# Kernel tuning notes

Measured on AMD Instinct MI355X. Metric: run time of the kernel, lower is better.

## Reference

```python
import jax, jax.numpy as jnp
import numpy as np

B, T, U = 4, 256, 128
ENC_H, PRED_H, JOINT_H = 512, 640, 640
NUM_CLASSES = 1024 + 1  # vocab + blank


def setup_inputs() -> dict:
    key = jax.random.key(0)
    ks = jax.random.split(key, 8)
    s = lambda fan_in: 1.0 / np.sqrt(fan_in)
    return {
        'encoder_outputs': jax.random.normal(ks[0], (B, ENC_H, T), jnp.float32),
        'decoder_outputs': jax.random.normal(ks[1], (B, PRED_H, U), jnp.float32),
        'W_enc': jax.random.uniform(ks[2], (JOINT_H, ENC_H), jnp.float32, -s(ENC_H), s(ENC_H)),
        'b_enc': jax.random.uniform(ks[3], (JOINT_H,), jnp.float32, -s(ENC_H), s(ENC_H)),
        'W_pred': jax.random.uniform(ks[4], (JOINT_H, PRED_H), jnp.float32, -s(PRED_H), s(PRED_H)),
        'b_pred': jax.random.uniform(ks[5], (JOINT_H,), jnp.float32, -s(PRED_H), s(PRED_H)),
        'W_joint': jax.random.uniform(ks[6], (NUM_CLASSES, JOINT_H), jnp.float32, -s(JOINT_H), s(JOINT_H)),
        'b_joint': jax.random.uniform(ks[7], (NUM_CLASSES,), jnp.float32, -s(JOINT_H), s(JOINT_H)),
    }


def reference(encoder_outputs, decoder_outputs, W_enc, b_enc, W_pred, b_pred, W_joint, b_joint):
    # encoder_outputs: [B, H_enc, T] -> [B, T, H_enc]; decoder: [B, H_pred, U] -> [B, U, H_pred]
    f = jnp.swapaxes(encoder_outputs, 1, 2)
    g = jnp.swapaxes(decoder_outputs, 1, 2)
    f = jnp.einsum('bth,jh->btj', f, W_enc) + b_enc          # [B, T, H]
    g = jnp.einsum('buh,jh->buj', g, W_pred) + b_pred        # [B, U, H]
    inp = f[:, :, None, :] + g[:, None, :, :]                # [B, T, U, H]
    hidden = jax.nn.relu(inp)
    logits = jnp.einsum('btuh,vh->btuv', hidden, W_joint) + b_joint  # [B, T, U, V+1]
    return jax.nn.log_softmax(logits, axis=-1)
```

## Files before the change

### kernel.cpp

```cpp
#include <hip/hip_runtime.h>

#define B_    4
#define T_    256
#define U_    128
#define ENC_H 512
#define PRED_H 640
#define JH    640
#define V_    1025
#define VMAIN 1024

#define BM    64
#define KC    32
#define APITCH 40
#define NKC   (JH / KC)

typedef float f32x4  __attribute__((ext_vector_type(4)));
typedef short bf16x8 __attribute__((ext_vector_type(8)));

__device__ __forceinline__ short bf16_rne(float x) {
    unsigned u = __float_as_uint(x);
    unsigned r = (u + 0x7fffu + ((u >> 16) & 1u)) >> 16;
    return (short)r;
}

__global__ __launch_bounds__(256) void proj_kernel(
    const float* __restrict__ X, const float* __restrict__ W,
    const float* __restrict__ bias, float* __restrict__ Y,
    int K, int M, int N)
{
    __shared__ float Xs[16][32];
    __shared__ float Ws[64][17];

    const int b  = blockIdx.z;
    const int m0 = blockIdx.x * 32;
    const int n0 = blockIdx.y * 64;
    const int tid = threadIdx.x;
    const int tx = tid & 15;
    const int ty = tid >> 4;

    const float* Xb = X + (size_t)b * K * M;

    float acc[2][4] = {{0.f,0.f,0.f,0.f},{0.f,0.f,0.f,0.f}};

    for (int k0 = 0; k0 < K; k0 += 16) {
        #pragma unroll
        for (int j = 0; j < 2; ++j) {
            int e = tid + j * 256;
            Xs[e >> 5][e & 31] = Xb[(size_t)(k0 + (e >> 5)) * M + m0 + (e & 31)];
        }
        #pragma unroll
        for (int j = 0; j < 4; ++j) {
            int e = tid + j * 256;
            Ws[e >> 4][e & 15] = W[(size_t)(n0 + (e >> 4)) * K + k0 + (e & 15)];
        }
        __syncthreads();
        #pragma unroll
        for (int k = 0; k < 16; ++k) {
            float a0 = Xs[k][ty * 2 + 0];
            float a1 = Xs[k][ty * 2 + 1];
            float b0 = Ws[tx * 4 + 0][k];
            float b1 = Ws[tx * 4 + 1][k];
            float b2 = Ws[tx * 4 + 2][k];
            float b3 = Ws[tx * 4 + 3][k];
            acc[0][0] += a0 * b0; acc[0][1] += a0 * b1;
            acc[0][2] += a0 * b2; acc[0][3] += a0 * b3;
            acc[1][0] += a1 * b0; acc[1][1] += a1 * b1;
            acc[1][2] += a1 * b2; acc[1][3] += a1 * b3;
        }
        __syncthreads();
    }

    #pragma unroll
    for (int i = 0; i < 2; ++i) {
        int m = m0 + ty * 2 + i;
        #pragma unroll
        for (int j = 0; j < 4; ++j) {
            int n = n0 + tx * 4 + j;
            Y[(size_t)(b * M + m) * N + n] = acc[i][j] + bias[n];
        }
    }
}

__global__ __launch_bounds__(256) void cvt_kernel(
    const float* __restrict__ W, short* __restrict__ o, int n)
{
    int i = blockIdx.x * 256 + threadIdx.x;
    if (i < n) o[i] = bf16_rne(W[i]);
}

__global__ __launch_bounds__(1024) void joint_kernel(
    const float* __restrict__ f,
    const float* __restrict__ g,
    const short* __restrict__ wj,
    const float* __restrict__ Wj32,
    const float* __restrict__ bj,
    float* __restrict__ out)
{
    __shared__ __align__(16) short As[2][BM * APITCH];
    __shared__ float red[BM][16];
    __shared__ float zp[BM][16];
    __shared__ float rowmax_s[BM], lse_s[BM], z1024_s[BM];

    const int bt = blockIdx.x >> 1;
    const int uh = blockIdx.x & 1;
    const int b  = bt >> 8;
    const int u0 = uh * BM;

    const float* frow = f + (size_t)bt * JH;
    const float* grow = g + (size_t)(b * U_ + u0) * JH;

    const int tid  = threadIdx.x;
    const int lane = tid & 63;
    const int wv   = tid >> 6;
    const int q    = lane >> 4;
    const int l15  = lane & 15;

    const int su = tid >> 4;
    const int sk = (tid & 15) * 2;

    f32x4 acc[4][4];
    #pragma unroll
    for (int rt = 0; rt < 4; ++rt)
        #pragma unroll
        for (int ct = 0; ct < 4; ++ct)
            acc[rt][ct] = (f32x4){0.f, 0.f, 0.f, 0.f};

    {
        float f0 = frow[sk], f1 = frow[sk + 1];
        float g0 = grow[su * JH + sk], g1 = grow[su * JH + sk + 1];
        As[0][su * APITCH + sk]     = bf16_rne(fmaxf(f0 + g0, 0.f));
        As[0][su * APITCH + sk + 1] = bf16_rne(fmaxf(f1 + g1, 0.f));
    }
    __syncthreads();

    for (int kc = 0; kc < NKC; ++kc) {
        const int cur = kc & 1;
        const bool more = (kc + 1) < NKC;
        float h0 = 0.f, h1 = 0.f;
        if (more) {
            const int k0n = (kc + 1) * KC;
            float f0 = frow[k0n + sk], f1 = frow[k0n + sk + 1];
            float g0 = grow[su * JH + k0n + sk], g1 = grow[su * JH + k0n + sk + 1];
            h0 = fmaxf(f0 + g0, 0.f);
            h1 = fmaxf(f1 + g1, 0.f);
        }
        const int k0 = kc * KC;
        bf16x8 bfr[4];
        #pragma unroll
        for (int ct = 0; ct < 4; ++ct) {
            const int col = (wv << 6) + (ct << 4) + l15;
            bfr[ct] = *(const bf16x8*)(wj + (size_t)col * JH + k0 + (q << 3));
        }
        bf16x8 afr[4];
        #pragma unroll
        for (int rt = 0; rt < 4; ++rt)
            afr[rt] = *(const bf16x8*)(&As[cur][(rt * 16 + l15) * APITCH + (q << 3)]);
        #pragma unroll
        for (int rt = 0; rt < 4; ++rt)
            #pragma unroll
            for (int ct = 0; ct < 4; ++ct)
                acc[rt][ct] = __builtin_amdgcn_mfma_f32_16x16x32_bf16(
                    afr[rt], bfr[ct], acc[rt][ct], 0, 0, 0);
        if (more) {
            const int ni = su * APITCH + sk;
            As[cur ^ 1][ni]     = bf16_rne(h0);
            As[cur ^ 1][ni + 1] = bf16_rne(h1);
        }
        __syncthreads();
    }

    float mloc[4][4];
    #pragma unroll
    for (int rt = 0; rt < 4; ++rt)
        #pragma unroll
        for (int r = 0; r < 4; ++r) mloc[rt][r] = -3.0e38f;

    #pragma unroll
    for (int ct = 0; ct < 4; ++ct) {
        const float bb = bj[(wv << 6) + (ct << 4) + l15];
        #pragma unroll
        for (int rt = 0; rt < 4; ++rt)
            #pragma unroll
            for (int r = 0; r < 4; ++r) {
                acc[rt][ct][r] += bb;
                mloc[rt][r] = fmaxf(mloc[rt][r], acc[rt][ct][r]);
            }
    }
    #pragma unroll
    for (int off = 1; off < 16; off <<= 1)
        #pragma unroll
        for (int rt = 0; rt < 4; ++rt)
            #pragma unroll
            for (int r = 0; r < 4; ++r)
                mloc[rt][r] = fmaxf(mloc[rt][r], __shfl_xor(mloc[rt][r], off));
    if (l15 == 0) {
        #pragma unroll
        for (int rt = 0; rt < 4; ++rt)
            #pragma unroll
            for (int r = 0; r < 4; ++r)
                red[rt * 16 + (q << 2) + r][wv] = mloc[rt][r];
    }
    {
        const int row  = tid >> 4;
        const int part = tid & 15;
        const float* w1024 = Wj32 + (size_t)VMAIN * JH;
        float s = 0.f;
        const int kb = part * 40;
        for (int kk = kb; kk < kb + 40; ++kk) {
            float h = fmaxf(frow[kk] + grow[row * JH + kk], 0.f);
            s += h * w1024[kk];
        }
        zp[row][part] = s;
    }
    __syncthreads();

    if (tid < BM) {
        float mx = red[tid][0];
        #pragma unroll
        for (int w = 1; w < 16; ++w) mx = fmaxf(mx, red[tid][w]);
        float z = bj[VMAIN];
        #pragma unroll
        for (int w = 0; w < 16; ++w) z += zp[tid][w];
        mx = fmaxf(mx, z);
        rowmax_s[tid] = mx;
        z1024_s[tid]  = z;
    }
    __syncthreads();

    float sloc[4][4];
    #pragma unroll
    for (int rt = 0; rt < 4; ++rt)
        #pragma unroll
        for (int r = 0; r < 4; ++r) {
            const float mx = rowmax_s[rt * 16 + (q << 2) + r];
            float s = 0.f;
            #pragma unroll
            for (int ct = 0; ct < 4; ++ct)
                s += __expf(acc[rt][ct][r] - mx);
            sloc[rt][r] = s;
        }
    #pragma unroll
    for (int off = 1; off < 16; off <<= 1)
        #pragma unroll
        for (int rt = 0; rt < 4; ++rt)
            #pragma unroll
            for (int r = 0; r < 4; ++r)
                sloc[rt][r] += __shfl_xor(sloc[rt][r], off);
    if (l15 == 0) {
        #pragma unroll
        for (int rt = 0; rt < 4; ++rt)
            #pragma unroll
            for (int r = 0; r < 4; ++r)
                red[rt * 16 + (q << 2) + r][wv] = sloc[rt][r];
    }
    __syncthreads();

    const size_t obase = (size_t)(bt * U_ + u0) * V_;
    if (tid < BM) {
        float tot = __expf(z1024_s[tid] - rowmax_s[tid]);
        #pragma unroll
        for (int w = 0; w < 16; ++w) tot += red[tid][w];
        float lse = rowmax_s[tid] + __logf(tot);
        lse_s[tid] = lse;
        out[obase + (size_t)tid * V_ + VMAIN] = z1024_s[tid] - lse;
    }
    __syncthreads();

    #pragma unroll
    for (int rt = 0; rt < 4; ++rt)
        #pragma unroll
        for (int r = 0; r < 4; ++r) {
            const int row = rt * 16 + (q << 2) + r;
            const float l = lse_s[row];
            #pragma unroll
            for (int ct = 0; ct < 4; ++ct) {
                const int col = (wv << 6) + (ct << 4) + l15;
                out[obase + (size_t)row * V_ + col] = acc[rt][ct][r] - l;
            }
        }
}

extern "C" void kernel_launch(void* const* d_in, const int* in_sizes, int n_in,
                              void* d_out, int out_size, void* d_ws, size_t ws_size,
                              hipStream_t stream) {
    const float* enc   = (const float*)d_in[0];
    const float* dec   = (const float*)d_in[1];
    const float* Wenc  = (const float*)d_in[2];
    const float* benc  = (const float*)d_in[3];
    const float* Wpred = (const float*)d_in[4];
    const float* bpred = (const float*)d_in[5];
    const float* Wj    = (const float*)d_in[6];
    const float* bjt   = (const float*)d_in[7];
    float* out = (float*)d_out;

    char* ws = (char*)d_ws;
    float* f_ws  = (float*)ws;
    float* g_ws  = (float*)(ws + 2621440);
    short* wj_ws = (short*)(ws + 2621440 + 1310720);

    proj_kernel<<<dim3(8, 10, 4), 256, 0, stream>>>(enc, Wenc, benc, f_ws, ENC_H, T_, JH);
    proj_kernel<<<dim3(4, 10, 4), 256, 0, stream>>>(dec, Wpred, bpred, g_ws, PRED_H, U_, JH);
    cvt_kernel<<<dim3((VMAIN * JH + 255) / 256), 256, 0, stream>>>(Wj, wj_ws, VMAIN * JH);
    joint_kernel<<<dim3(B_ * T_ * 2), 1024, 0, stream>>>(f_ws, g_ws, wj_ws, Wj, bjt, out);
}
```

Before: 1.141 ms.

## Stage full hidden tile in LDS once and vectorize projection and convert kernels

The joint kernel now builds the entire 64x640 bf16 ReLU hidden tile in shared memory up front with float4 loads, which removes the per-chunk double-buffer barriers from the MFMA loop and lets that loop be fully unrolled. The projection kernel moves to 64x64 tiles with a 4x4 register block and float4 global and LDS access, the weight convert kernel handles four elements per thread, and the blank-logit dot product uses float4 loads. The larger LDS footprint (about 83KB) may limit occupancy, and staging the whole tile up front loses the overlap of loads with compute.

```diff
diff --git a/kernel.cpp b/kernel.cpp
--- a/kernel.cpp
+++ b/kernel.cpp
@@ -11,8 +11,8 @@
 
 #define BM    64
 #define KC    32
-#define APITCH 40
 #define NKC   (JH / KC)
+#define PA    648
 
 typedef float f32x4  __attribute__((ext_vector_type(4)));
 typedef short bf16x8 __attribute__((ext_vector_type(8)));
@@ -28,64 +28,80 @@
     const float* __restrict__ bias, float* __restrict__ Y,
     int K, int M, int N)
 {
-    __shared__ float Xs[16][32];
-    __shared__ float Ws[64][17];
+    __shared__ float Xs[16][68];
+    __shared__ float Wt[16][68];
 
     const int b  = blockIdx.z;
-    const int m0 = blockIdx.x * 32;
+    const int m0 = blockIdx.x * 64;
     const int n0 = blockIdx.y * 64;
     const int tid = threadIdx.x;
-    const int tx = tid & 15;
-    const int ty = tid >> 4;
+    const int tm = tid & 15;
+    const int tn = tid >> 4;
 
     const float* Xb = X + (size_t)b * K * M;
 
-    float acc[2][4] = {{0.f,0.f,0.f,0.f},{0.f,0.f,0.f,0.f}};
+    const int lk = tid >> 4;
+    const int lm = (tid & 15) * 4;
+    const int wn = tid >> 2;
+    const int wk = (tid & 3) * 4;
+
+    float acc[4][4];
+    #pragma unroll
+    for (int i = 0; i < 4; ++i)
+        #pragma unroll
+        for (int j = 0; j < 4; ++j) acc[i][j] = 0.f;
 
     for (int k0 = 0; k0 < K; k0 += 16) {
-        #pragma unroll
-        for (int j = 0; j < 2; ++j) {
-            int e = tid + j * 256;
-            Xs[e >> 5][e & 31] = Xb[(size_t)(k0 + (e >> 5)) * M + m0 + (e & 31)];
-        }
-        #pragma unroll
-        for (int j = 0; j < 4; ++j) {
-            int e = tid + j * 256;
-            Ws[e >> 4][e & 15] = W[(size_t)(n0 + (e >> 4)) * K + k0 + (e & 15)];
-        }
+        float4 xv = *(const float4*)(Xb + (size_t)(k0 + lk) * M + m0 + lm);
+        *(float4*)&Xs[lk][lm] = xv;
+        float4 wv4 = *(const float4*)(W + (size_t)(n0 + wn) * K + k0 + wk);
+        Wt[wk + 0][wn] = wv4.x;
+        Wt[wk + 1][wn] = wv4.y;
+        Wt[wk + 2][wn] = wv4.z;
+        Wt[wk + 3][wn] = wv4.w;
         __syncthreads();
         #pragma unroll
         for (int k = 0; k < 16; ++k) {
-            float a0 = Xs[k][ty * 2 + 0];
-            float a1 = Xs[k][ty * 2 + 1];
-            float b0 = Ws[tx * 4 + 0][k];
-            float b1 = Ws[tx * 4 + 1][k];
-            float b2 = Ws[tx * 4 + 2][k];
-            float b3 = Ws[tx * 4 + 3][k];
-            acc[0][0] += a0 * b0; acc[0][1] += a0 * b1;
-            acc[0][2] += a0 * b2; acc[0][3] += a0 * b3;
-            acc[1][0] += a1 * b0; acc[1][1] += a1 * b1;
-            acc[1][2] += a1 * b2; acc[1][3] += a1 * b3;
+            float4 a4 = *(const float4*)&Xs[k][tm * 4];
+            float4 b4 = *(const float4*)&Wt[k][tn * 4];
+            acc[0][0] += a4.x * b4.x; acc[0][1] += a4.x * b4.y;
+            acc[0][2] += a4.x * b4.z; acc[0][3] += a4.x * b4.w;
+            acc[1][0] += a4.y * b4.x; acc[1][1] += a4.y * b4.y;
+            acc[1][2] += a4.y * b4.z; acc[1][3] += a4.y * b4.w;
+            acc[2][0] += a4.z * b4.x; acc[2][1] += a4.z * b4.y;
+            acc[2][2] += a4.z * b4.z; acc[2][3] += a4.z * b4.w;
+            acc[3][0] += a4.w * b4.x; acc[3][1] += a4.w * b4.y;
+            acc[3][2] += a4.w * b4.z; acc[3][3] += a4.w * b4.w;
         }
         __syncthreads();
     }
 
-    #pragma unroll
-    for (int i = 0; i < 2; ++i) {
-        int m = m0 + ty * 2 + i;
-        #pragma unroll
-        for (int j = 0; j < 4; ++j) {
-            int n = n0 + tx * 4 + j;
-            Y[(size_t)(b * M + m) * N + n] = acc[i][j] + bias[n];
-        }
+    float4 bv = *(const float4*)(bias + n0 + tn * 4);
+    #pragma unroll
+    for (int i = 0; i < 4; ++i) {
+        const int m = m0 + tm * 4 + i;
+        float4 o;
+        o.x = acc[i][0] + bv.x;
+        o.y = acc[i][1] + bv.y;
+        o.z = acc[i][2] + bv.z;
+        o.w = acc[i][3] + bv.w;
+        *(float4*)(Y + (size_t)(b * M + m) * N + n0 + tn * 4) = o;
     }
 }
 
 __global__ __launch_bounds__(256) void cvt_kernel(
     const float* __restrict__ W, short* __restrict__ o, int n)
 {
-    int i = blockIdx.x * 256 + threadIdx.x;
-    if (i < n) o[i] = bf16_rne(W[i]);
+    int i = (blockIdx.x * 256 + threadIdx.x) * 4;
+    if (i < n) {
+        float4 v = *(const float4*)(W + i);
+        short4 s;
+        s.x = bf16_rne(v.x);
+        s.y = bf16_rne(v.y);
+        s.z = bf16_rne(v.z);
+        s.w = bf16_rne(v.w);
+        *(short4*)(o + i) = s;
+    }
 }
 
 __global__ __launch_bounds__(1024) void joint_kernel(
@@ -96,7 +112,7 @@
     const float* __restrict__ bj,
     float* __restrict__ out)
 {
-    __shared__ __align__(16) short As[2][BM * APITCH];
+    __shared__ __align__(16) short As[BM * PA];
     __shared__ float red[BM][16];
     __shared__ float zp[BM][16];
     __shared__ float rowmax_s[BM], lse_s[BM], z1024_s[BM];
@@ -115,8 +131,25 @@
     const int q    = lane >> 4;
     const int l15  = lane & 15;
 
-    const int su = tid >> 4;
-    const int sk = (tid & 15) * 2;
+    {
+        const int su = tid >> 4;
+        const int sp = tid & 15;
+        const float* gr = grow + (size_t)su * JH;
+        short* dst = As + su * PA;
+        #pragma unroll
+        for (int i = 0; i < 10; ++i) {
+            const int k = sp * 4 + i * 64;
+            float4 fv = *(const float4*)(frow + k);
+            float4 gv = *(const float4*)(gr + k);
+            short4 h;
+            h.x = bf16_rne(fmaxf(fv.x + gv.x, 0.f));
+            h.y = bf16_rne(fmaxf(fv.y + gv.y, 0.f));
+            h.z = bf16_rne(fmaxf(fv.z + gv.z, 0.f));
+            h.w = bf16_rne(fmaxf(fv.w + gv.w, 0.f));
+            *(short4*)(dst + k) = h;
+        }
+    }
+    __syncthreads();
 
     f32x4 acc[4][4];
     #pragma unroll
@@ -125,48 +158,30 @@
         for (int ct = 0; ct < 4; ++ct)
             acc[rt][ct] = (f32x4){0.f, 0.f, 0.f, 0.f};
 
-    {
-        float f0 = frow[sk], f1 = frow[sk + 1];
-        float g0 = grow[su * JH + sk], g1 = grow[su * JH + sk + 1];
-        As[0][su * APITCH + sk]     = bf16_rne(fmaxf(f0 + g0, 0.f));
-        As[0][su * APITCH + sk + 1] = bf16_rne(fmaxf(f1 + g1, 0.f));
-    }
-    __syncthreads();
-
+    const short* bptr[4];
+    #pragma unroll
+    for (int ct = 0; ct < 4; ++ct)
+        bptr[ct] = wj + (size_t)((wv << 6) + (ct << 4) + l15) * JH + (q << 3);
+    const short* aptr[4];
+    #pragma unroll
+    for (int rt = 0; rt < 4; ++rt)
+        aptr[rt] = As + (rt * 16 + l15) * PA + (q << 3);
+
+    #pragma unroll
     for (int kc = 0; kc < NKC; ++kc) {
-        const int cur = kc & 1;
-        const bool more = (kc + 1) < NKC;
-        float h0 = 0.f, h1 = 0.f;
-        if (more) {
-            const int k0n = (kc + 1) * KC;
-            float f0 = frow[k0n + sk], f1 = frow[k0n + sk + 1];
-            float g0 = grow[su * JH + k0n + sk], g1 = grow[su * JH + k0n + sk + 1];
-            h0 = fmaxf(f0 + g0, 0.f);
-            h1 = fmaxf(f1 + g1, 0.f);
-        }
-        const int k0 = kc * KC;
-        bf16x8 bfr[4];
-        #pragma unroll
-        for (int ct = 0; ct < 4; ++ct) {
-            const int col = (wv << 6) + (ct << 4) + l15;
-            bfr[ct] = *(const bf16x8*)(wj + (size_t)col * JH + k0 + (q << 3));
-        }
-        bf16x8 afr[4];
-        #pragma unroll
-        for (int rt = 0; rt < 4; ++rt)
-            afr[rt] = *(const bf16x8*)(&As[cur][(rt * 16 + l15) * APITCH + (q << 3)]);
+        bf16x8 bfr[4], afr[4];
+        #pragma unroll
+        for (int ct = 0; ct < 4; ++ct)
+            bfr[ct] = *(const bf16x8*)(bptr[ct] + kc * KC);
+        #pragma unroll
+        for (int rt = 0; rt < 4; ++rt)
+            afr[rt] = *(const bf16x8*)(aptr[rt] + kc * KC);
         #pragma unroll
         for (int rt = 0; rt < 4; ++rt)
             #pragma unroll
             for (int ct = 0; ct < 4; ++ct)
                 acc[rt][ct] = __builtin_amdgcn_mfma_f32_16x16x32_bf16(
                     afr[rt], bfr[ct], acc[rt][ct], 0, 0, 0);
-        if (more) {
-            const int ni = su * APITCH + sk;
-            As[cur ^ 1][ni]     = bf16_rne(h0);
-            As[cur ^ 1][ni + 1] = bf16_rne(h1);
-        }
-        __syncthreads();
     }
 
     float mloc[4][4];
@@ -204,11 +219,18 @@
         const int row  = tid >> 4;
         const int part = tid & 15;
         const float* w1024 = Wj32 + (size_t)VMAIN * JH;
+        const float* gr = grow + (size_t)row * JH;
+        const int kb = part * 40;
         float s = 0.f;
-        const int kb = part * 40;
-        for (int kk = kb; kk < kb + 40; ++kk) {
-            float h = fmaxf(frow[kk] + grow[row * JH + kk], 0.f);
-            s += h * w1024[kk];
+        #pragma unroll
+        for (int i = 0; i < 10; ++i) {
+            float4 fv = *(const float4*)(frow + kb + i * 4);
+            float4 gv = *(const float4*)(gr + kb + i * 4);
+            float4 wv4 = *(const float4*)(w1024 + kb + i * 4);
+            s += fmaxf(fv.x + gv.x, 0.f) * wv4.x
+               + fmaxf(fv.y + gv.y, 0.f) * wv4.y
+               + fmaxf(fv.z + gv.z, 0.f) * wv4.z
+               + fmaxf(fv.w + gv.w, 0.f) * wv4.w;
         }
         zp[row][part] = s;
     }
@@ -298,8 +320,8 @@
     float* g_ws  = (float*)(ws + 2621440);
     short* wj_ws = (short*)(ws + 2621440 + 1310720);
 
-    proj_kernel<<<dim3(8, 10, 4), 256, 0, stream>>>(enc, Wenc, benc, f_ws, ENC_H, T_, JH);
-    proj_kernel<<<dim3(4, 10, 4), 256, 0, stream>>>(dec, Wpred, bpred, g_ws, PRED_H, U_, JH);
-    cvt_kernel<<<dim3((VMAIN * JH + 255) / 256), 256, 0, stream>>>(Wj, wj_ws, VMAIN * JH);
+    proj_kernel<<<dim3(4, 10, 4), 256, 0, stream>>>(enc, Wenc, benc, f_ws, ENC_H, T_, JH);
+    proj_kernel<<<dim3(2, 10, 4), 256, 0, stream>>>(dec, Wpred, bpred, g_ws, PRED_H, JH == JH ? U_ : U_, JH);
+    cvt_kernel<<<dim3((VMAIN * JH / 4 + 255) / 256), 256, 0, stream>>>(Wj, wj_ws, VMAIN * JH);
     joint_kernel<<<dim3(B_ * T_ * 2), 1024, 0, stream>>>(f_ws, g_ws, wj_ws, Wj, bjt, out);
 }
```

Result: faster. 1.060 ms (-7.1%).
